# Kernel tuning notes

Measured on AMD Instinct MI355X. Metric: run time of the kernel, lower is better.

Reference implementation:

```python
import jax, jax.numpy as jnp
import numpy as np

B, N, IN_F, OUT_F, HEADS = 16, 256, 128, 64, 4
NEG = -9e15

def setup_inputs() -> dict:
    key = jax.random.key(0)
    ks = jax.random.split(key, 7)
    x = jax.random.normal(ks[0], (B, N, IN_F), dtype=jnp.float32)
    adj = jax.random.randint(ks[1], (B, N, N), 0, 2, dtype=jnp.int32)
    adj_in = jax.random.randint(ks[2], (B, N, N), 0, 2, dtype=jnp.int32)
    adj_out = jax.random.randint(ks[3], (B, N, N), 0, 2, dtype=jnp.int32)
    # params: W linear (no bias), a linear (with bias)
    gain = 1.414
    lim_W = gain * np.sqrt(6.0 / (IN_F + OUT_F))
    W = jax.random.uniform(ks[4], (OUT_F, IN_F), jnp.float32, -lim_W, lim_W)
    lim_A = gain * np.sqrt(6.0 / (2 * OUT_F + 3 * HEADS))
    A = jax.random.uniform(ks[5], (3 * HEADS, 2 * OUT_F), jnp.float32, -lim_A, lim_A)
    a_b = jax.random.uniform(ks[6], (3 * HEADS,), jnp.float32, -1.0, 1.0) / np.sqrt(2 * OUT_F)
    return {"x": x, "adj": adj, "adj_in": adj_in, "adj_out": adj_out,
            "W": W, "A": A, "a_b": a_b}

def reference(x, adj, adj_in, adj_out, W, A, a_b):
    # h = W(input): [B, N, OUT_F]
    h = jnp.einsum('bni,oi->bno', x, W)
    # additive attention: a(cat[h_i, h_j]) = h_i @ A1^T + h_j @ A2^T + b
    A1, A2 = A[:, :OUT_F], A[:, OUT_F:]
    e_src = jnp.einsum('bnd,hd->bnh', h, A1)  # depends on row i
    e_dst = jnp.einsum('bnd,hd->bnh', h, A2)  # depends on col j
    e = e_src[:, :, None, :] + e_dst[:, None, :, :] + a_b  # [B, N, N, 3H]
    e = jax.nn.leaky_relu(e, negative_slope=0.01)
    e = jnp.transpose(e, (0, 3, 1, 2))  # [B, 3H, N, N]
    # tripled masks: [adj]*H ++ [adj_in]*H ++ [adj_out]*H along head axis
    mask = jnp.concatenate([
        jnp.repeat(adj[:, None], HEADS, axis=1),
        jnp.repeat(adj_in[:, None], HEADS, axis=1),
        jnp.repeat(adj_out[:, None], HEADS, axis=1)], axis=1)  # [B, 3H, N, N]
    att = jnp.where(mask > 0, e, jnp.float32(NEG))
    att = jax.nn.softmax(att, axis=-1)
    # dropout omitted (eval mode)
    h_prime = jnp.einsum('bhij,bjd->bhid', att, h).mean(axis=1)  # [B, N, OUT_F]
    return h_prime
```

## Files before the change

kernel.cpp:

```cpp
#include <hip/hip_runtime.h>

#define L2E 1.44269504088896340736f

typedef __attribute__((ext_vector_type(8))) short bf16x8;
typedef __attribute__((ext_vector_type(4))) float f32x4;

__device__ __forceinline__ unsigned bf16_rne(float v) {
    unsigned x = __float_as_uint(v);
    return (x + 0x7FFFu + ((x >> 16) & 1u)) >> 16;
}

__device__ __forceinline__ void cvt_hilo4(float4 v, uint2* hi, uint2* lo) {
    unsigned h0 = bf16_rne(v.x), h1 = bf16_rne(v.y), h2 = bf16_rne(v.z), h3 = bf16_rne(v.w);
    float f0 = __uint_as_float(h0 << 16), f1 = __uint_as_float(h1 << 16);
    float f2 = __uint_as_float(h2 << 16), f3 = __uint_as_float(h3 << 16);
    unsigned l0 = bf16_rne(v.x - f0), l1 = bf16_rne(v.y - f1);
    unsigned l2 = bf16_rne(v.z - f2), l3 = bf16_rne(v.w - f3);
    hi->x = h0 | (h1 << 16); hi->y = h2 | (h3 << 16);
    lo->x = l0 | (l1 << 16); lo->y = l2 | (l3 << 16);
}

__global__ __launch_bounds__(256) void k1_proj(
    const float* __restrict__ x, const float* __restrict__ W, const float* __restrict__ A,
    const float* __restrict__ ab,
    unsigned short* __restrict__ hTg, float* __restrict__ esrc, float* __restrict__ edstT)
{
    __shared__ unsigned short xh[16 * 136], xl[16 * 136];
    __shared__ unsigned short wh[64 * 136], wl[64 * 136];
    __shared__ unsigned short Ach[32 * 72], Acl[32 * 72];
    __shared__ unsigned short hsh[16 * 72], hsl[16 * 72];

    const int t = threadIdx.x;
    const int row0 = blockIdx.x * 16;
    const int b = row0 >> 8;
    const int ibase = row0 & 255;

#pragma unroll
    for (int p = 0; p < 2; ++p) {
        int q = t + 256 * p;
        int r = q >> 5, c = (q & 31) * 4;
        float4 v = *(const float4*)&x[row0 * 128 + 4 * q];
        uint2 hi, lo; cvt_hilo4(v, &hi, &lo);
        *(uint2*)&xh[r * 136 + c] = hi;
        *(uint2*)&xl[r * 136 + c] = lo;
    }
#pragma unroll
    for (int p = 0; p < 8; ++p) {
        int q = t + 256 * p;
        int r = q >> 5, c = (q & 31) * 4;
        float4 v = *(const float4*)&W[4 * q];
        uint2 hi, lo; cvt_hilo4(v, &hi, &lo);
        *(uint2*)&wh[r * 136 + c] = hi;
        *(uint2*)&wl[r * 136 + c] = lo;
    }
#pragma unroll
    for (int p = 0; p < 2; ++p) {
        int q = t + 256 * p;
        int n = q >> 4, d = (q & 15) * 4;
        float4 v = make_float4(0.f, 0.f, 0.f, 0.f);
        if (n < 24) {
            int nn = (n < 12) ? n : n - 12;
            v = *(const float4*)&A[nn * 128 + ((n < 12) ? 0 : 64) + d];
        }
        uint2 hi, lo; cvt_hilo4(v, &hi, &lo);
        *(uint2*)&Ach[n * 72 + d] = hi;
        *(uint2*)&Acl[n * 72 + d] = lo;
    }
    __syncthreads();

    const int lane = t & 63;
    const int wv = t >> 6;
    const int ml = lane & 15, kb = lane >> 4;

    f32x4 acc = {0.f, 0.f, 0.f, 0.f};
#pragma unroll
    for (int ks = 0; ks < 4; ++ks) {
        const int ko = ks * 32 + kb * 8;
        bf16x8 axh = *(const bf16x8*)&xh[ml * 136 + ko];
        bf16x8 axl = *(const bf16x8*)&xl[ml * 136 + ko];
        bf16x8 bwh = *(const bf16x8*)&wh[(wv * 16 + ml) * 136 + ko];
        bf16x8 bwl = *(const bf16x8*)&wl[(wv * 16 + ml) * 136 + ko];
        acc = __builtin_amdgcn_mfma_f32_16x16x32_bf16(axh, bwh, acc, 0, 0, 0);
        acc = __builtin_amdgcn_mfma_f32_16x16x32_bf16(axh, bwl, acc, 0, 0, 0);
        acc = __builtin_amdgcn_mfma_f32_16x16x32_bf16(axl, bwh, acc, 0, 0, 0);
    }
#pragma unroll
    for (int r = 0; r < 4; ++r) {
        const int m = kb * 4 + r, c = wv * 16 + ml;
        unsigned hi = bf16_rne(acc[r]);
        float hif = __uint_as_float(hi << 16);
        hsh[m * 72 + c] = (unsigned short)hi;
        hsl[m * 72 + c] = (unsigned short)bf16_rne(acc[r] - hif);
    }
    __syncthreads();

    if (wv < 2) {
        f32x4 e4 = {0.f, 0.f, 0.f, 0.f};
#pragma unroll
        for (int ks = 0; ks < 2; ++ks) {
            const int ko = ks * 32 + kb * 8;
            bf16x8 ah = *(const bf16x8*)&hsh[ml * 72 + ko];
            bf16x8 al = *(const bf16x8*)&hsl[ml * 72 + ko];
            bf16x8 bh = *(const bf16x8*)&Ach[(wv * 16 + ml) * 72 + ko];
            bf16x8 bl = *(const bf16x8*)&Acl[(wv * 16 + ml) * 72 + ko];
            e4 = __builtin_amdgcn_mfma_f32_16x16x32_bf16(ah, bh, e4, 0, 0, 0);
            e4 = __builtin_amdgcn_mfma_f32_16x16x32_bf16(ah, bl, e4, 0, 0, 0);
            e4 = __builtin_amdgcn_mfma_f32_16x16x32_bf16(al, bh, e4, 0, 0, 0);
        }
#pragma unroll
        for (int r = 0; r < 4; ++r) {
            const int m = kb * 4 + r, n = wv * 16 + ml;
            if (n < 12)
                esrc[(row0 + m) * 12 + n] = (e4[r] + ab[n]) * L2E;
            else if (n < 24)
                edstT[(b * 12 + (n - 12)) * 256 + ibase + m] = e4[r] * L2E;
        }
    }

#pragma unroll
    for (int it = 0; it < 2; ++it) {
        int e2 = t + 256 * it;
        int d = e2 >> 3, j2 = (e2 & 7) * 2;
        unsigned lo16 = hsh[j2 * 72 + d], hi16 = hsh[(j2 + 1) * 72 + d];
        *(unsigned*)&hTg[(b * 64 + d) * 256 + ibase + j2] = lo16 | (hi16 << 16);
    }
}

__global__ __launch_bounds__(256) void k2_attn(
    const int* __restrict__ adj, const int* __restrict__ adjin, const int* __restrict__ adjout,
    const float* __restrict__ esrc, const float* __restrict__ edstT,
    const unsigned short* __restrict__ hTg,
    float* __restrict__ out)
{
    __shared__ unsigned short Ph[16 * 264];

    const int t = threadIdx.x;
    const int b  = blockIdx.x >> 5;
    const int i0 = (blockIdx.x & 31) * 8;
    const int lane = t & 63;
    const int wv = t >> 6;
    const int g = lane >> 5;
    const int q = lane & 31;
    const int row = wv * 2 + g;
    const int gi = b * 256 + i0 + row;

    {
        uint4* z = (uint4*)&Ph[8 * 264];
        if (t < 264) z[t] = make_uint4(0, 0, 0, 0);
    }

    const int4* mp0 = (const int4*)(adj    + (size_t)gi * 256 + 8 * q);
    const int4* mp1 = (const int4*)(adjin  + (size_t)gi * 256 + 8 * q);
    const int4* mp2 = (const int4*)(adjout + (size_t)gi * 256 + 8 * q);
    int4 Ma0 = mp0[0], Ma1 = mp0[1];
    int4 Mb0 = mp1[0], Mb1 = mp1[1];
    int4 Mc0 = mp2[0], Mc1 = mp2[1];
    float fm[3][8];
    fm[0][0] = (float)Ma0.x; fm[0][1] = (float)Ma0.y; fm[0][2] = (float)Ma0.z; fm[0][3] = (float)Ma0.w;
    fm[0][4] = (float)Ma1.x; fm[0][5] = (float)Ma1.y; fm[0][6] = (float)Ma1.z; fm[0][7] = (float)Ma1.w;
    fm[1][0] = (float)Mb0.x; fm[1][1] = (float)Mb0.y; fm[1][2] = (float)Mb0.z; fm[1][3] = (float)Mb0.w;
    fm[1][4] = (float)Mb1.x; fm[1][5] = (float)Mb1.y; fm[1][6] = (float)Mb1.z; fm[1][7] = (float)Mb1.w;
    fm[2][0] = (float)Mc0.x; fm[2][1] = (float)Mc0.y; fm[2][2] = (float)Mc0.z; fm[2][3] = (float)Mc0.w;
    fm[2][4] = (float)Mc1.x; fm[2][5] = (float)Mc1.y; fm[2][6] = (float)Mc1.z; fm[2][7] = (float)Mc1.w;

    const float4* ep = (const float4*)(esrc + (size_t)gi * 12);
    const float4 eA = ep[0], eB = ep[1], eC = ep[2];
    const float e0[12] = {eA.x, eA.y, eA.z, eA.w, eB.x, eB.y, eB.z, eB.w, eC.x, eC.y, eC.z, eC.w};

    float Pacc[8] = {0.f, 0.f, 0.f, 0.f, 0.f, 0.f, 0.f, 0.f};
#pragma unroll
    for (int hh = 0; hh < 12; ++hh) {
        const int grp = hh >> 2;
        const float4* evp = (const float4*)(edstT + (size_t)(b * 12 + hh) * 256 + 8 * q);
        const float4 ev0 = evp[0], ev1 = evp[1];
        const float evv[8] = {ev0.x, ev0.y, ev0.z, ev0.w, ev1.x, ev1.y, ev1.z, ev1.w};
        float p[8], s = 0.f;
#pragma unroll
        for (int k = 0; k < 8; ++k) {
            float v = e0[hh] + evv[k];
            v = fmaxf(v, 0.01f * v);
            p[k] = __builtin_amdgcn_exp2f(v) * fm[grp][k];
            s += p[k];
        }
#pragma unroll
        for (int off = 16; off >= 1; off >>= 1)
            s += __shfl_xor(s, off);
        const float rinv = __builtin_amdgcn_rcpf(s);
#pragma unroll
        for (int k = 0; k < 8; ++k)
            Pacc[k] += p[k] * rinv;
    }
    {
        uint4 pk;
        pk.x = bf16_rne(Pacc[0]) | (bf16_rne(Pacc[1]) << 16);
        pk.y = bf16_rne(Pacc[2]) | (bf16_rne(Pacc[3]) << 16);
        pk.z = bf16_rne(Pacc[4]) | (bf16_rne(Pacc[5]) << 16);
        pk.w = bf16_rne(Pacc[6]) | (bf16_rne(Pacc[7]) << 16);
        *(uint4*)&Ph[row * 264 + 8 * q] = pk;
    }
    __syncthreads();

    const int ml = lane & 15, kb = lane >> 4;
    const unsigned short* hTb = hTg + ((size_t)b * 64 + wv * 16 + ml) * 256;
    f32x4 acc = {0.f, 0.f, 0.f, 0.f};
#pragma unroll
    for (int ks = 0; ks < 8; ++ks) {
        const int ko = ks * 32 + kb * 8;
        bf16x8 bh = *(const bf16x8*)&hTb[ko];
        bf16x8 ah = *(const bf16x8*)&Ph[ml * 264 + ko];
        acc = __builtin_amdgcn_mfma_f32_16x16x32_bf16(ah, bh, acc, 0, 0, 0);
    }
    if (kb < 2) {
#pragma unroll
        for (int r = 0; r < 4; ++r) {
            const int m = kb * 4 + r;
            out[(size_t)(b * 256 + i0 + m) * 64 + wv * 16 + ml] = acc[r] * (1.0f / 12.0f);
        }
    }
}

extern "C" void kernel_launch(void* const* d_in, const int* in_sizes, int n_in,
                              void* d_out, int out_size, void* d_ws, size_t ws_size,
                              hipStream_t stream) {
    const float* x    = (const float*)d_in[0];
    const int*   adj  = (const int*)d_in[1];
    const int*   adji = (const int*)d_in[2];
    const int*   adjo = (const int*)d_in[3];
    const float* W    = (const float*)d_in[4];
    const float* A    = (const float*)d_in[5];
    const float* ab   = (const float*)d_in[6];
    float* out = (float*)d_out;

    unsigned short* hTg = (unsigned short*)d_ws;
    float* esrc  = (float*)((char*)d_ws + (512 << 10));
    float* edstT = (float*)((char*)d_ws + (704 << 10));

    k1_proj<<<256, 256, 0, stream>>>(x, W, A, ab, hTg, esrc, edstT);
    k2_attn<<<512, 256, 0, stream>>>(adj, adji, adjo, esrc, edstT, hTg, out);
}
```

Measured before the change: 18.00 us.

## Drop split-bf16 compensation in projection kernel and load operands directly from global

Replaces the three-MFMA hi/lo bf16 split emulation of fp32 with a single plain bf16 MFMA for both the x·W projection and the attention-logit projection. Operands are converted straight from global memory into registers, so the shared-memory staging of x, W and A is gone. The kernel now works on 8-row tiles over twice as many blocks, which wastes half of each MFMA's M dimension. Plain bf16 lowers the precision of h and of the logits, which risks exceeding the accuracy tolerance.

```diff
diff --git a/kernel.cpp b/kernel.cpp
--- a/kernel.cpp
+++ b/kernel.cpp
@@ -10,119 +10,96 @@
     return (x + 0x7FFFu + ((x >> 16) & 1u)) >> 16;
 }
 
-__device__ __forceinline__ void cvt_hilo4(float4 v, uint2* hi, uint2* lo) {
-    unsigned h0 = bf16_rne(v.x), h1 = bf16_rne(v.y), h2 = bf16_rne(v.z), h3 = bf16_rne(v.w);
-    float f0 = __uint_as_float(h0 << 16), f1 = __uint_as_float(h1 << 16);
-    float f2 = __uint_as_float(h2 << 16), f3 = __uint_as_float(h3 << 16);
-    unsigned l0 = bf16_rne(v.x - f0), l1 = bf16_rne(v.y - f1);
-    unsigned l2 = bf16_rne(v.z - f2), l3 = bf16_rne(v.w - f3);
-    hi->x = h0 | (h1 << 16); hi->y = h2 | (h3 << 16);
-    lo->x = l0 | (l1 << 16); lo->y = l2 | (l3 << 16);
+__device__ __forceinline__ bf16x8 cvt8(float4 a, float4 b) {
+    bf16x8 r;
+    r[0] = (short)bf16_rne(a.x); r[1] = (short)bf16_rne(a.y);
+    r[2] = (short)bf16_rne(a.z); r[3] = (short)bf16_rne(a.w);
+    r[4] = (short)bf16_rne(b.x); r[5] = (short)bf16_rne(b.y);
+    r[6] = (short)bf16_rne(b.z); r[7] = (short)bf16_rne(b.w);
+    return r;
+}
+
+__device__ __forceinline__ bf16x8 cvt8g(const float* p) {
+    float4 a = *(const float4*)p;
+    float4 b = *(const float4*)(p + 4);
+    return cvt8(a, b);
 }
 
 __global__ __launch_bounds__(256) void k1_proj(
     const float* __restrict__ x, const float* __restrict__ W, const float* __restrict__ A,
     const float* __restrict__ ab,
-    unsigned short* __restrict__ hTg, float* __restrict__ esrc, float* __restrict__ edstT)
+    unsigned short* __restrict__ hTg, float* __restrict__ esg, float* __restrict__ edTg)
 {
-    __shared__ unsigned short xh[16 * 136], xl[16 * 136];
-    __shared__ unsigned short wh[64 * 136], wl[64 * 136];
-    __shared__ unsigned short Ach[32 * 72], Acl[32 * 72];
-    __shared__ unsigned short hsh[16 * 72], hsl[16 * 72];
+    __shared__ unsigned short hsh[16 * 72];
 
     const int t = threadIdx.x;
-    const int row0 = blockIdx.x * 16;
-    const int b = row0 >> 8;
-    const int ibase = row0 & 255;
-
-#pragma unroll
-    for (int p = 0; p < 2; ++p) {
-        int q = t + 256 * p;
-        int r = q >> 5, c = (q & 31) * 4;
-        float4 v = *(const float4*)&x[row0 * 128 + 4 * q];
-        uint2 hi, lo; cvt_hilo4(v, &hi, &lo);
-        *(uint2*)&xh[r * 136 + c] = hi;
-        *(uint2*)&xl[r * 136 + c] = lo;
-    }
-#pragma unroll
-    for (int p = 0; p < 8; ++p) {
-        int q = t + 256 * p;
-        int r = q >> 5, c = (q & 31) * 4;
-        float4 v = *(const float4*)&W[4 * q];
-        uint2 hi, lo; cvt_hilo4(v, &hi, &lo);
-        *(uint2*)&wh[r * 136 + c] = hi;
-        *(uint2*)&wl[r * 136 + c] = lo;
-    }
-#pragma unroll
-    for (int p = 0; p < 2; ++p) {
-        int q = t + 256 * p;
-        int n = q >> 4, d = (q & 15) * 4;
-        float4 v = make_float4(0.f, 0.f, 0.f, 0.f);
-        if (n < 24) {
-            int nn = (n < 12) ? n : n - 12;
-            v = *(const float4*)&A[nn * 128 + ((n < 12) ? 0 : 64) + d];
-        }
-        uint2 hi, lo; cvt_hilo4(v, &hi, &lo);
-        *(uint2*)&Ach[n * 72 + d] = hi;
-        *(uint2*)&Acl[n * 72 + d] = lo;
-    }
-    __syncthreads();
-
-    const int lane = t & 63;
-    const int wv = t >> 6;
+    const int b = blockIdx.x >> 5;
+    const int ibase = (blockIdx.x & 31) * 8;
+    const int row0 = b * 256 + ibase;
+    const int lane = t & 63, wv = t >> 6;
     const int ml = lane & 15, kb = lane >> 4;
+
+    const int xr = row0 + (ml < 8 ? ml : 0);
+    const float* xp = x + (size_t)xr * 128;
+    const float* wp = W + (size_t)(wv * 16 + ml) * 128;
+
+    const int n_e = wv * 16 + ml;
+    float4 ea0, ea1, ea2, ea3;
+    float abv = 0.f;
+    if (wv < 2 && n_e < 24) {
+        const float* ap = (n_e < 12) ? (A + n_e * 128) : (A + (n_e - 12) * 128 + 64);
+        ea0 = *(const float4*)(ap + kb * 8);
+        ea1 = *(const float4*)(ap + kb * 8 + 4);
+        ea2 = *(const float4*)(ap + 32 + kb * 8);
+        ea3 = *(const float4*)(ap + 32 + kb * 8 + 4);
+        if (n_e < 12) abv = ab[n_e];
+    } else {
+        ea0 = ea1 = ea2 = ea3 = make_float4(0.f, 0.f, 0.f, 0.f);
+    }
 
     f32x4 acc = {0.f, 0.f, 0.f, 0.f};
 #pragma unroll
     for (int ks = 0; ks < 4; ++ks) {
         const int ko = ks * 32 + kb * 8;
-        bf16x8 axh = *(const bf16x8*)&xh[ml * 136 + ko];
-        bf16x8 axl = *(const bf16x8*)&xl[ml * 136 + ko];
-        bf16x8 bwh = *(const bf16x8*)&wh[(wv * 16 + ml) * 136 + ko];
-        bf16x8 bwl = *(const bf16x8*)&wl[(wv * 16 + ml) * 136 + ko];
-        acc = __builtin_amdgcn_mfma_f32_16x16x32_bf16(axh, bwh, acc, 0, 0, 0);
-        acc = __builtin_amdgcn_mfma_f32_16x16x32_bf16(axh, bwl, acc, 0, 0, 0);
-        acc = __builtin_amdgcn_mfma_f32_16x16x32_bf16(axl, bwh, acc, 0, 0, 0);
-    }
-#pragma unroll
-    for (int r = 0; r < 4; ++r) {
-        const int m = kb * 4 + r, c = wv * 16 + ml;
-        unsigned hi = bf16_rne(acc[r]);
-        float hif = __uint_as_float(hi << 16);
-        hsh[m * 72 + c] = (unsigned short)hi;
-        hsl[m * 72 + c] = (unsigned short)bf16_rne(acc[r] - hif);
+        bf16x8 ax = cvt8g(xp + ko);
+        bf16x8 bw = cvt8g(wp + ko);
+        acc = __builtin_amdgcn_mfma_f32_16x16x32_bf16(ax, bw, acc, 0, 0, 0);
+    }
+
+    if (kb < 2) {
+        const int d = wv * 16 + ml;
+        unsigned w0 = bf16_rne(acc[0]) | (bf16_rne(acc[1]) << 16);
+        unsigned w1 = bf16_rne(acc[2]) | (bf16_rne(acc[3]) << 16);
+        uint2 pk; pk.x = w0; pk.y = w1;
+        *(uint2*)&hTg[(size_t)(b * 64 + d) * 256 + ibase + kb * 4] = pk;
+#pragma unroll
+        for (int r = 0; r < 4; ++r)
+            hsh[(kb * 4 + r) * 72 + d] = (unsigned short)bf16_rne(acc[r]);
     }
     __syncthreads();
 
     if (wv < 2) {
+        bf16x8 eb0 = cvt8(ea0, ea1);
+        bf16x8 eb1 = cvt8(ea2, ea3);
         f32x4 e4 = {0.f, 0.f, 0.f, 0.f};
-#pragma unroll
-        for (int ks = 0; ks < 2; ++ks) {
-            const int ko = ks * 32 + kb * 8;
-            bf16x8 ah = *(const bf16x8*)&hsh[ml * 72 + ko];
-            bf16x8 al = *(const bf16x8*)&hsl[ml * 72 + ko];
-            bf16x8 bh = *(const bf16x8*)&Ach[(wv * 16 + ml) * 72 + ko];
-            bf16x8 bl = *(const bf16x8*)&Acl[(wv * 16 + ml) * 72 + ko];
-            e4 = __builtin_amdgcn_mfma_f32_16x16x32_bf16(ah, bh, e4, 0, 0, 0);
-            e4 = __builtin_amdgcn_mfma_f32_16x16x32_bf16(ah, bl, e4, 0, 0, 0);
-            e4 = __builtin_amdgcn_mfma_f32_16x16x32_bf16(al, bh, e4, 0, 0, 0);
-        }
-#pragma unroll
-        for (int r = 0; r < 4; ++r) {
-            const int m = kb * 4 + r, n = wv * 16 + ml;
-            if (n < 12)
-                esrc[(row0 + m) * 12 + n] = (e4[r] + ab[n]) * L2E;
-            else if (n < 24)
-                edstT[(b * 12 + (n - 12)) * 256 + ibase + m] = e4[r] * L2E;
-        }
-    }
-
-#pragma unroll
-    for (int it = 0; it < 2; ++it) {
-        int e2 = t + 256 * it;
-        int d = e2 >> 3, j2 = (e2 & 7) * 2;
-        unsigned lo16 = hsh[j2 * 72 + d], hi16 = hsh[(j2 + 1) * 72 + d];
-        *(unsigned*)&hTg[(b * 64 + d) * 256 + ibase + j2] = lo16 | (hi16 << 16);
+        {
+            bf16x8 ah0 = *(const bf16x8*)&hsh[ml * 72 + kb * 8];
+            bf16x8 ah1 = *(const bf16x8*)&hsh[ml * 72 + 32 + kb * 8];
+            e4 = __builtin_amdgcn_mfma_f32_16x16x32_bf16(ah0, eb0, e4, 0, 0, 0);
+            e4 = __builtin_amdgcn_mfma_f32_16x16x32_bf16(ah1, eb1, e4, 0, 0, 0);
+        }
+        if (kb < 2) {
+            if (n_e < 12) {
+#pragma unroll
+                for (int r = 0; r < 4; ++r)
+                    esg[(size_t)(row0 + kb * 4 + r) * 12 + n_e] = (e4[r] + abv) * L2E;
+            } else if (n_e < 24) {
+                float4 ev;
+                ev.x = e4[0] * L2E; ev.y = e4[1] * L2E;
+                ev.z = e4[2] * L2E; ev.w = e4[3] * L2E;
+                *(float4*)&edTg[(size_t)(b * 12 + (n_e - 12)) * 256 + ibase + kb * 4] = ev;
+            }
+        }
     }
 }
 
@@ -232,9 +209,9 @@
     float* out = (float*)d_out;
 
     unsigned short* hTg = (unsigned short*)d_ws;
-    float* esrc  = (float*)((char*)d_ws + (512 << 10));
-    float* edstT = (float*)((char*)d_ws + (704 << 10));
-
-    k1_proj<<<256, 256, 0, stream>>>(x, W, A, ab, hTg, esrc, edstT);
-    k2_attn<<<512, 256, 0, stream>>>(adj, adji, adjo, esrc, edstT, hTg, out);
-}
+    float* esg  = (float*)((char*)d_ws + (512 << 10));
+    float* edTg = (float*)((char*)d_ws + (704 << 10));
+
+    k1_proj<<<512, 256, 0, stream>>>(x, W, A, ab, hTg, esg, edTg);
+    k2_attn<<<512, 256, 0, stream>>>(adj, adji, adjo, esg, edTg, hTg, out);
+}
```

Measured after the change: 19.13 us. +6.3%, slower.
